# Optimization experiments

Hardware: AMD Instinct MI355X
Metric: run time of the kernel (lower is better)

## Reference

```python
import jax, jax.numpy as jnp
import numpy as np

B, C, H, W = 4, 256, 128, 128
D = 256            # attention hidden_dim (== C, so no output_proj)
HID = 1024         # mlp hidden = int(C * 4.0)
EPS = 1e-5


def setup_inputs() -> dict:
    key = jax.random.key(0)
    ks = jax.random.split(key, 16)
    s = 0.02
    return {
        "x": jax.random.normal(ks[0], (B, C, H, W), jnp.float32),
        "wq": jax.random.normal(ks[1], (C, D), jnp.float32) * s,
        "bq": jnp.zeros((D,), jnp.float32),
        "wk": jax.random.normal(ks[2], (C, D), jnp.float32) * s,
        "bk": jnp.zeros((D,), jnp.float32),
        "wv": jax.random.normal(ks[3], (C, D), jnp.float32) * s,
        "bv": jnp.zeros((D,), jnp.float32),
        "ln1_g": jnp.ones((C,), jnp.float32),
        "ln1_b": jnp.zeros((C,), jnp.float32),
        "ln2_g": jnp.ones((C,), jnp.float32),
        "ln2_b": jnp.zeros((C,), jnp.float32),
        "fc1_w": jax.random.normal(ks[4], (C, HID), jnp.float32) * s,
        "fc1_b": jnp.zeros((HID,), jnp.float32),
        "fc2_w": jax.random.normal(ks[5], (HID, C), jnp.float32) * s,
        "fc2_b": jnp.zeros((C,), jnp.float32),
    }


def _layernorm(x, g, b):
    m = jnp.mean(x, axis=-1, keepdims=True)
    v = jnp.mean(jnp.square(x - m), axis=-1, keepdims=True)
    return (x - m) * jax.lax.rsqrt(v + EPS) * g + b


def _neighborhoods(t):
    # t: [B,H,W,D] -> [B,H,W,9,D] 3x3 neighborhoods, zero-padded at borders
    tp = jnp.pad(t, ((0, 0), (1, 1), (1, 1), (0, 0)))
    h, w = t.shape[1], t.shape[2]
    return jnp.stack(
        [tp[:, dy:dy + h, dx:dx + w, :] for dy in range(3) for dx in range(3)],
        axis=3,
    )


def _valid_mask(h, w):
    # [H,W,9] bool: which of the 9 neighbors are inside the grid
    ys = jnp.arange(h)[:, None] * jnp.ones((1, w), jnp.int32)
    xs = jnp.arange(w)[None, :] * jnp.ones((h, 1), jnp.int32)
    top, bot = ys > 0, ys < h - 1
    lef, rig = xs > 0, xs < w - 1
    ones = jnp.ones((h, w), bool)
    return jnp.stack(
        [top & lef, top, top & rig, lef, ones, rig, bot & lef, bot, bot & rig],
        axis=-1,
    )


def reference(x, wq, bq, wk, bk, wv, bv, ln1_g, ln1_b, ln2_g, ln2_b,
              fc1_w, fc1_b, fc2_w, fc2_b):
    b_, c_, h_, w_ = x.shape
    xc = jnp.transpose(x, (0, 2, 3, 1))                    # [B,H,W,C]
    n1 = _layernorm(xc, ln1_g, ln1_b)
    q = n1 @ wq + bq                                       # [B,H,W,D]
    k = n1 @ wk + bk
    v = n1 @ wv + bv
    kn = _neighborhoods(k)                                  # [B,H,W,9,D]
    vn = _neighborhoods(v)
    scores = jnp.einsum('bhwd,bhwnd->bhwn', q, kn) / jnp.sqrt(jnp.float32(q.shape[-1]))
    mask = _valid_mask(h_, w_)                               # [H,W,9]
    scores = jnp.where(mask, scores, jnp.float32(-1e9))
    weights = jax.nn.softmax(scores, axis=-1)
    attn = jnp.einsum('bhwn,bhwnd->bhwd', weights, vn)       # [B,H,W,D]
    x1 = xc + attn                                           # residual 1
    n2 = _layernorm(x1, ln2_g, ln2_b)
    mlp = jax.nn.gelu(n2 @ fc1_w + fc1_b, approximate=False) @ fc2_w + fc2_b
    out = x1 + mlp
    return jnp.transpose(out, (0, 3, 1, 2))                  # [B,C,H,W]
```

## Files before the change

### kernel.cpp

```cpp
#include <hip/hip_runtime.h>
#include <hip/hip_bf16.h>
#include <math.h>

#define NPIX  65536
#define CCH   256
#define HWSZ  16384
#define WIDTH 128
#define HID   1024

typedef unsigned short u16;
typedef __bf16 bf16x8 __attribute__((ext_vector_type(8)));
typedef float  floatx4 __attribute__((ext_vector_type(4)));

__device__ __forceinline__ float bf2f(u16 u) {
  union { unsigned int i; float f; } c; c.i = ((unsigned int)u) << 16; return c.f;
}
__device__ __forceinline__ float bflo(unsigned int u) {
  union { unsigned int i; float f; } c; c.i = u << 16; return c.f;
}
__device__ __forceinline__ float bfhi(unsigned int u) {
  union { unsigned int i; float f; } c; c.i = u & 0xffff0000u; return c.f;
}
__device__ __forceinline__ u16 f2bf(float f) {
  union { float f; unsigned int i; } c; c.f = f;
  unsigned int x = c.i;
  x += 0x7fffu + ((x >> 16) & 1u);
  return (u16)(x >> 16);
}
__device__ __forceinline__ unsigned int packbf(float lo, float hi) {
  return ((unsigned int)f2bf(hi) << 16) | (unsigned int)f2bf(lo);
}
__device__ __forceinline__ float fast_rcp(float x) {
  float r; asm("v_rcp_f32 %0, %1" : "=v"(r) : "v"(x)); return r;
}
__device__ __forceinline__ float fast_exp2(float x) {
  float r; asm("v_exp_f32 %0, %1" : "=v"(r) : "v"(x)); return r;
}
__device__ __forceinline__ float gelu_fast(float x) {
  const float u = x * x;
  const float s = x * fmaf(0.1029432f, u, 2.3022082f);
  const float e = fast_exp2(-s);
  return x * fast_rcp(1.0f + e);
}

__device__ __forceinline__ void async16(const void* g, void* l) {
  __builtin_amdgcn_global_load_lds(
      (const __attribute__((address_space(1))) void*)g,
      (__attribute__((address_space(3))) void*)l, 16, 0, 0);
}

__global__ __launch_bounds__(256) void wfrag_kernel(
    const float* __restrict__ src, u16* __restrict__ dst, int N, int K) {
  const int tid = threadIdx.x;
  const int u = blockIdx.x * 4 + (tid >> 6);
  const int lane = tid & 63, quad = lane >> 4, l16 = lane & 15;
  const int K32 = K >> 5;
  const int g = u / K32, kb = u - g * K32;
  const int n = g * 16 + l16;
  const int k0 = kb * 32 + quad * 8;
  u16 tmp[8];
#pragma unroll
  for (int e = 0; e < 8; e++) tmp[e] = f2bf(src[(size_t)(k0 + e) * N + n]);
  *(bf16x8*)(dst + ((size_t)u * 64 + lane) * 8) = *(bf16x8*)tmp;
}

__global__ __launch_bounds__(256) void concat_bias_kernel(
    const float* __restrict__ bq, const float* __restrict__ bk,
    const float* __restrict__ bv, float* __restrict__ dst) {
  const int i = blockIdx.x * 256 + threadIdx.x;
  if (i < 256) dst[i] = bq[i];
  else if (i < 512) dst[i] = bk[i - 256];
  else if (i < 768) dst[i] = bv[i - 512];
}

__global__ __launch_bounds__(256) void ln1_kernel(
    const float* __restrict__ x, const float* __restrict__ g,
    const float* __restrict__ bb, u16* __restrict__ n1) {
  __shared__ float sx[32][257];
  __shared__ float sred[16][32];
  __shared__ float sm[32], sr[32];
  const int tx = threadIdx.x;
  const int p0 = blockIdx.x * 32;
  {
    const int pix = tx & 31, cpart = tx >> 5;
    const int p = p0 + pix;
    const int b = p >> 14, hw = p & (HWSZ - 1);
    const float* xb = x + ((size_t)b * CCH) * HWSZ + hw;
    float s = 0.f, s2 = 0.f;
#pragma unroll 4
    for (int i = 0; i < 32; i++) {
      const int c = cpart * 32 + i;
      const float v = xb[(size_t)c * HWSZ];
      sx[pix][c] = v;
      s += v; s2 += v * v;
    }
    sred[cpart][pix] = s; sred[8 + cpart][pix] = s2;
  }
  __syncthreads();
  if (tx < 32) {
    float s = 0.f, s2 = 0.f;
#pragma unroll
    for (int j = 0; j < 8; j++) { s += sred[j][tx]; s2 += sred[8 + j][tx]; }
    const float m = s * (1.0f / 256.0f);
    const float var = s2 * (1.0f / 256.0f) - m * m;
    sm[tx] = m; sr[tx] = rsqrtf(var + 1e-5f);
  }
  __syncthreads();
  const float gc = g[tx], bc = bb[tx];
#pragma unroll 4
  for (int i = 0; i < 32; i++) {
    const float v = (sx[i][tx] - sm[i]) * sr[i] * gc + bc;
    n1[(size_t)(p0 + i) * CCH + tx] = f2bf(v);
  }
}

__global__ __launch_bounds__(256) void res_ln2_kernel(
    const float* __restrict__ x, const u16* __restrict__ attn,
    const float* __restrict__ g, const float* __restrict__ bb,
    float* __restrict__ x1, u16* __restrict__ n2) {
  __shared__ float sx[32][257];
  __shared__ float sred[16][32];
  __shared__ float sm[32], sr[32];
  const int tx = threadIdx.x;
  const int p0 = blockIdx.x * 32;
  {
    const int pix = tx & 31, cpart = tx >> 5;
    const int p = p0 + pix;
    const int b = p >> 14, hw = p & (HWSZ - 1);
    const float* xb = x + ((size_t)b * CCH) * HWSZ + hw;
#pragma unroll 4
    for (int i = 0; i < 32; i++) {
      const int c = cpart * 32 + i;
      sx[pix][c] = xb[(size_t)c * HWSZ];
    }
  }
  __syncthreads();
#pragma unroll 4
  for (int i = 0; i < 32; i++) {
    const float v = sx[i][tx] + bf2f(attn[(size_t)(p0 + i) * CCH + tx]);
    sx[i][tx] = v;
    x1[(size_t)(p0 + i) * CCH + tx] = v;
  }
  __syncthreads();
  {
    const int pix = tx & 31, cpart = tx >> 5;
    float s = 0.f, s2 = 0.f;
#pragma unroll 4
    for (int i = 0; i < 32; i++) {
      const float v = sx[pix][cpart * 32 + i];
      s += v; s2 += v * v;
    }
    sred[cpart][pix] = s; sred[8 + cpart][pix] = s2;
  }
  __syncthreads();
  if (tx < 32) {
    float s = 0.f, s2 = 0.f;
#pragma unroll
    for (int j = 0; j < 8; j++) { s += sred[j][tx]; s2 += sred[8 + j][tx]; }
    const float m = s * (1.0f / 256.0f);
    const float var = s2 * (1.0f / 256.0f) - m * m;
    sm[tx] = m; sr[tx] = rsqrtf(var + 1e-5f);
  }
  __syncthreads();
  const float gc = g[tx], bc = bb[tx];
#pragma unroll 4
  for (int i = 0; i < 32; i++) {
    const float v = (sx[i][tx] - sm[i]) * sr[i] * gc + bc;
    n2[(size_t)(p0 + i) * CCH + tx] = f2bf(v);
  }
}

__global__ __launch_bounds__(256) void attn_kernel(
    const u16* __restrict__ qkv, u16* __restrict__ attn) {
  const int tid = threadIdx.x;
  const int wave = tid >> 6, lane = tid & 63;
  const int p = blockIdx.x * 4 + wave;
  const int hw = p & (HWSZ - 1);
  const int hh = hw >> 7, ww = hw & (WIDTH - 1);
  const u16* rowp = qkv + (size_t)p * 768 + lane * 4;
  const uint2 qr = *(const uint2*)rowp;
  const float qf0 = bflo(qr.x), qf1 = bfhi(qr.x);
  const float qf2 = bflo(qr.y), qf3 = bfhi(qr.y);
  float sc[9];
#pragma unroll
  for (int n = 0; n < 9; n++) {
    const int dy = n / 3 - 1, dx = n % 3 - 1;
    const int y = hh + dy, x2 = ww + dx;
    float s = -1e30f;
    if (y >= 0 && y < 128 && x2 >= 0 && x2 < 128) {
      const uint2 kr = *(const uint2*)(rowp + 256 + (dy * WIDTH + dx) * 768);
      float d = qf0 * bflo(kr.x) + qf1 * bfhi(kr.x)
              + qf2 * bflo(kr.y) + qf3 * bfhi(kr.y);
#pragma unroll
      for (int o = 32; o >= 1; o >>= 1) d += __shfl_xor(d, o, 64);
      s = d * 0.0625f;
    }
    sc[n] = s;
  }
  float mx = sc[0];
#pragma unroll
  for (int n = 1; n < 9; n++) mx = fmaxf(mx, sc[n]);
  float wgt[9], wsum = 0.f;
#pragma unroll
  for (int n = 0; n < 9; n++) { wgt[n] = __expf(sc[n] - mx); wsum += wgt[n]; }
  const float inv = 1.0f / wsum;
  float a0 = 0.f, a1 = 0.f, a2 = 0.f, a3 = 0.f;
#pragma unroll
  for (int n = 0; n < 9; n++) {
    const int dy = n / 3 - 1, dx = n % 3 - 1;
    const int y = hh + dy, x2 = ww + dx;
    if (y >= 0 && y < 128 && x2 >= 0 && x2 < 128) {
      const uint2 vr = *(const uint2*)(rowp + 512 + (dy * WIDTH + dx) * 768);
      const float wn = wgt[n] * inv;
      a0 += wn * bflo(vr.x); a1 += wn * bfhi(vr.x);
      a2 += wn * bflo(vr.y); a3 += wn * bfhi(vr.y);
    }
  }
  uint2 o;
  o.x = ((unsigned int)f2bf(a1) << 16) | (unsigned int)f2bf(a0);
  o.y = ((unsigned int)f2bf(a3) << 16) | (unsigned int)f2bf(a2);
  *(uint2*)(attn + (size_t)p * CCH + lane * 4) = o;
}

template <int NCH, int NST, int EPI>
__global__ __launch_bounds__(256, 3) void gemm_blds(
    const u16* __restrict__ A, const u16* __restrict__ wf,
    const float* __restrict__ bias, u16* __restrict__ outb) {
  __shared__ u16 sB[2][16384];
  const int tid  = threadIdx.x;
  const int wave = tid >> 6, lane = tid & 63;
  const int quad = lane >> 4, l16 = lane & 15;
  const int m0 = blockIdx.x * 128 + wave * 32;

  const u16* aRow = A + (size_t)(m0 + l16) * CCH + quad * 8;
  bf16x8 afr[2][8];
#pragma unroll
  for (int mi = 0; mi < 2; mi++)
#pragma unroll
    for (int ks = 0; ks < 8; ks++)
      afr[mi][ks] = *(const bf16x8*)(aRow + (size_t)mi * 16 * CCH + ks * 32);

  u16* rowPtr0 = outb + (size_t)(m0 + l16) * NST;
  u16* rowPtr1 = rowPtr0 + (size_t)16 * NST;

  auto stage = [&](int ch, int buf) {
    const u16* g = wf + (size_t)ch * 16384;
#pragma unroll
    for (int i = 0; i < 8; i++)
      async16(g + i * 2048 + tid * 8, &sB[buf][i * 2048 + tid * 8]);
  };

  stage(0, 0);
#pragma unroll 1
  for (int ch = 0; ch < NCH; ++ch) {
    __syncthreads();
    if (ch + 1 < NCH) stage(ch + 1, (ch + 1) & 1);
    const u16* sb = sB[ch & 1];
    floatx4 acc[2][4];
#pragma unroll
    for (int mi = 0; mi < 2; mi++)
#pragma unroll
      for (int gi = 0; gi < 4; gi++) acc[mi][gi] = (floatx4){0.f, 0.f, 0.f, 0.f};
#pragma unroll
    for (int ks = 0; ks < 8; ks++) {
      bf16x8 bfr[4];
#pragma unroll
      for (int gi = 0; gi < 4; gi++)
        bfr[gi] = *(const bf16x8*)&sb[(gi * 8 + ks) * 512 + lane * 8];
#pragma unroll
      for (int mi = 0; mi < 2; mi++)
#pragma unroll
        for (int gi = 0; gi < 4; gi++)
          acc[mi][gi] = __builtin_amdgcn_mfma_f32_16x16x32_bf16(
              bfr[gi], afr[mi][ks], acc[mi][gi], 0, 0, 0);
    }
#pragma unroll
    for (int gi = 0; gi < 4; gi++) {
      const int colb = ch * 64 + gi * 16 + quad * 4;
      const floatx4 bs4 = *(const floatx4*)&bias[colb];
#pragma unroll
      for (int mi = 0; mi < 2; mi++) {
        float v[4];
#pragma unroll
        for (int r = 0; r < 4; r++) {
          float val = acc[mi][gi][r] + bs4[r];
          if constexpr (EPI == 1) val = gelu_fast(val);
          v[r] = val;
        }
        uint2 w;
        w.x = packbf(v[0], v[1]);
        w.y = packbf(v[2], v[3]);
        *(uint2*)((mi == 0 ? rowPtr0 : rowPtr1) + colb) = w;
      }
    }
  }
}

__global__ __launch_bounds__(256, 2) void fc2_kernel(
    const u16* __restrict__ h, const u16* __restrict__ f2F,
    const float* __restrict__ bias, const float* __restrict__ x1,
    float* __restrict__ out) {
  __shared__ u16 sA[4][4096];
  __shared__ u16 sB[4][4096];
  const int tid  = threadIdx.x;
  const int wave = tid >> 6, lane = tid & 63;
  const int quad = lane >> 4, l16 = lane & 15;
  const int bx = blockIdx.x;
  const int mblk = (bx >> 1) * 128;
  const int nb = bx & 1;
  const int wgi = (wave >> 1) * 4;
  const int mloc = (wave & 1) * 64;

  auto stageA = [&](int kc, int buf) {
#pragma unroll
    for (int i = 0; i < 2; i++) {
      const int s = i * 256 + tid;
      async16(h + (size_t)(mblk + (s >> 2)) * HID + kc * 32 + (s & 3) * 8,
              &sA[buf][s * 8]);
    }
  };
  auto stageB = [&](int kc, int buf) {
#pragma unroll
    for (int i = 0; i < 2; i++) {
      const int s = i * 256 + tid;
      async16(f2F + (((size_t)(nb * 8 + (s >> 6)) * 32 + kc) << 9) + (s & 63) * 8,
              &sB[buf][s * 8]);
    }
  };

  floatx4 acc[4][4];
#pragma unroll
  for (int mi = 0; mi < 4; mi++)
#pragma unroll
    for (int gi = 0; gi < 4; gi++) acc[mi][gi] = (floatx4){0.f, 0.f, 0.f, 0.f};

  stageA(0, 0); stageB(0, 0);
  stageA(1, 1); stageB(1, 1);
#pragma unroll 1
  for (int kc = 0; kc < 32; ++kc) {
    if (kc < 31) asm volatile("s_waitcnt vmcnt(4)" ::: "memory");
    else         asm volatile("s_waitcnt vmcnt(0)" ::: "memory");
    __builtin_amdgcn_s_barrier();
    __builtin_amdgcn_sched_barrier(0);
    if (kc + 2 < 32) { stageA(kc + 2, (kc + 2) & 3); stageB(kc + 2, (kc + 2) & 3); }
    const u16* sa = sA[kc & 3];
    const u16* sb = sB[kc & 3];
    bf16x8 bfr[4], afr[4];
#pragma unroll
    for (int gi = 0; gi < 4; gi++)
      bfr[gi] = *(const bf16x8*)&sb[(wgi + gi) * 512 + lane * 8];
#pragma unroll
    for (int mi = 0; mi < 4; mi++)
      afr[mi] = *(const bf16x8*)&sa[(mloc + mi * 16 + l16) * 32 + quad * 8];
#pragma unroll
    for (int mi = 0; mi < 4; mi++)
#pragma unroll
      for (int gi = 0; gi < 4; gi++)
        acc[mi][gi] = __builtin_amdgcn_mfma_f32_16x16x32_bf16(
            afr[mi], bfr[gi], acc[mi][gi], 0, 0, 0);
  }

  const int m0 = mblk + mloc;
#pragma unroll
  for (int mi = 0; mi < 4; mi++)
#pragma unroll
    for (int gi = 0; gi < 4; gi++) {
      const int col = nb * 128 + (wgi + gi) * 16 + l16;
      const float bs = bias[col];
      const int row0 = m0 + mi * 16 + quad * 4;
      floatx4 vv;
#pragma unroll
      for (int r = 0; r < 4; r++)
        vv[r] = acc[mi][gi][r] + bs + x1[(size_t)(row0 + r) * CCH + col];
      *(floatx4*)&out[((size_t)((row0 >> 14) * CCH + col)) * HWSZ + (row0 & (HWSZ - 1))] = vv;
    }
}

extern "C" void kernel_launch(void* const* d_in, const int* in_sizes, int n_in,
                              void* d_out, int out_size, void* d_ws, size_t ws_size,
                              hipStream_t stream) {
  const float* x    = (const float*)d_in[0];
  const float* wq   = (const float*)d_in[1];
  const float* bq   = (const float*)d_in[2];
  const float* wk   = (const float*)d_in[3];
  const float* bk   = (const float*)d_in[4];
  const float* wv   = (const float*)d_in[5];
  const float* bv   = (const float*)d_in[6];
  const float* ln1g = (const float*)d_in[7];
  const float* ln1b = (const float*)d_in[8];
  const float* ln2g = (const float*)d_in[9];
  const float* ln2b = (const float*)d_in[10];
  const float* fc1w = (const float*)d_in[11];
  const float* fc1b = (const float*)d_in[12];
  const float* fc2w = (const float*)d_in[13];
  const float* fc2b = (const float*)d_in[14];
  float* out = (float*)d_out;

  char* ws = (char*)d_ws;
  const size_t MB = (size_t)1 << 20;
  float* x1   = (float*)(ws);
  u16* qkv    = (u16*)(ws + 64 * MB);
  u16* hbuf   = (u16*)(ws + 64 * MB);
  u16* n1     = (u16*)(ws + 160 * MB);
  u16* attnb  = n1;
  u16* n2     = (u16*)(ws + 192 * MB);
  u16* wqkvF  = (u16*)(ws + 224 * MB);
  u16* f1F    = wqkvF + 768 * 256;
  u16* f2F    = f1F + 1024 * 256;
  float* bqkv = (float*)(f2F + 256 * 1024);

  dim3 blk(256);
  wfrag_kernel<<<dim3(32),  blk, 0, stream>>>(wq,   wqkvF,          256, 256);
  wfrag_kernel<<<dim3(32),  blk, 0, stream>>>(wk,   wqkvF + 65536,  256, 256);
  wfrag_kernel<<<dim3(32),  blk, 0, stream>>>(wv,   wqkvF + 131072, 256, 256);
  wfrag_kernel<<<dim3(128), blk, 0, stream>>>(fc1w, f1F, 1024, 256);
  wfrag_kernel<<<dim3(128), blk, 0, stream>>>(fc2w, f2F, 256, 1024);
  concat_bias_kernel<<<dim3(3), blk, 0, stream>>>(bq, bk, bv, bqkv);

  ln1_kernel<<<NPIX / 32, blk, 0, stream>>>(x, ln1g, ln1b, n1);

  gemm_blds<12, 768, 0><<<dim3(NPIX / 128), blk, 0, stream>>>(n1, wqkvF, bqkv, qkv);

  attn_kernel<<<NPIX / 4, blk, 0, stream>>>(qkv, attnb);

  res_ln2_kernel<<<NPIX / 32, blk, 0, stream>>>(x, attnb, ln2g, ln2b, x1, n2);

  gemm_blds<16, 1024, 1><<<dim3(NPIX / 128), blk, 0, stream>>>(n2, f1F, fc1b, hbuf);

  fc2_kernel<<<dim3((NPIX / 128) * 2), blk, 0, stream>>>(hbuf, f2F, fc2b, x1, out);
}
```

Baseline: 460.0 us.

## Fuse fc1+GELU+fc2 into one MLP kernel keeping hidden activations on-chip

Replaces the separate fc1 GEMM (writing a bf16 hidden buffer to global memory) and fc2 GEMM with a single kernel. Each wave computes a 16-row slab of GELU(fc1) for 64 hidden columns per chunk, passes it through a small LDS scratch, and accumulates fc2 directly in registers, with fc2 weights read straight from global memory. This removes the round trip of the large hidden activation. It costs more registers, lower M-tile reuse of the weights (64 rows per block), and uncached global weight loads in the inner loop. It also changes the QKV GEMM's barrier to a partial vmcnt wait and hoists its bias load ahead of the next stage's prefetch.

```diff
diff --git a/kernel.cpp b/kernel.cpp
--- a/kernel.cpp
+++ b/kernel.cpp
@@ -253,8 +253,16 @@
   stage(0, 0);
 #pragma unroll 1
   for (int ch = 0; ch < NCH; ++ch) {
-    __syncthreads();
+    if (ch == 0) asm volatile("s_waitcnt vmcnt(0)" ::: "memory");
+    else         asm volatile("s_waitcnt vmcnt(8)" ::: "memory");
+    __builtin_amdgcn_s_barrier();
+    __builtin_amdgcn_sched_barrier(0);
+    floatx4 bs4pre[4];
+#pragma unroll
+    for (int gi = 0; gi < 4; gi++)
+      bs4pre[gi] = *(const floatx4*)&bias[ch * 64 + gi * 16 + quad * 4];
     if (ch + 1 < NCH) stage(ch + 1, (ch + 1) & 1);
+    __builtin_amdgcn_sched_barrier(0);
     const u16* sb = sB[ch & 1];
     floatx4 acc[2][4];
 #pragma unroll
@@ -277,7 +285,7 @@
 #pragma unroll
     for (int gi = 0; gi < 4; gi++) {
       const int colb = ch * 64 + gi * 16 + quad * 4;
-      const floatx4 bs4 = *(const floatx4*)&bias[colb];
+      const floatx4 bs4 = bs4pre[gi];
 #pragma unroll
       for (int mi = 0; mi < 2; mi++) {
         float v[4];
@@ -296,84 +304,102 @@
   }
 }
 
-__global__ __launch_bounds__(256, 2) void fc2_kernel(
-    const u16* __restrict__ h, const u16* __restrict__ f2F,
-    const float* __restrict__ bias, const float* __restrict__ x1,
+__global__ __launch_bounds__(256, 2) void mlp_kernel(
+    const u16* __restrict__ n2, const u16* __restrict__ f1F,
+    const u16* __restrict__ f2F, const float* __restrict__ b1,
+    const float* __restrict__ b2, const float* __restrict__ x1,
     float* __restrict__ out) {
-  __shared__ u16 sA[4][4096];
-  __shared__ u16 sB[4][4096];
+  __shared__ u16 sW[2][16384];
+  __shared__ __align__(16) u16 hx[4][16][72];
   const int tid  = threadIdx.x;
   const int wave = tid >> 6, lane = tid & 63;
   const int quad = lane >> 4, l16 = lane & 15;
-  const int bx = blockIdx.x;
-  const int mblk = (bx >> 1) * 128;
-  const int nb = bx & 1;
-  const int wgi = (wave >> 1) * 4;
-  const int mloc = (wave & 1) * 64;
-
-  auto stageA = [&](int kc, int buf) {
-#pragma unroll
-    for (int i = 0; i < 2; i++) {
-      const int s = i * 256 + tid;
-      async16(h + (size_t)(mblk + (s >> 2)) * HID + kc * 32 + (s & 3) * 8,
-              &sA[buf][s * 8]);
-    }
+  const int m0w = blockIdx.x * 64 + wave * 16;
+
+  const u16* aRow = n2 + (size_t)(m0w + l16) * CCH + quad * 8;
+  bf16x8 afr[8];
+#pragma unroll
+  for (int ks = 0; ks < 8; ks++)
+    afr[ks] = *(const bf16x8*)(aRow + ks * 32);
+
+  auto stageW1 = [&](int hc, int buf) {
+    const u16* g = f1F + (size_t)hc * 16384;
+#pragma unroll
+    for (int i = 0; i < 8; i++)
+      async16(g + i * 2048 + tid * 8, &sW[buf][i * 2048 + tid * 8]);
   };
-  auto stageB = [&](int kc, int buf) {
-#pragma unroll
-    for (int i = 0; i < 2; i++) {
-      const int s = i * 256 + tid;
-      async16(f2F + (((size_t)(nb * 8 + (s >> 6)) * 32 + kc) << 9) + (s & 63) * 8,
-              &sB[buf][s * 8]);
-    }
-  };
-
-  floatx4 acc[4][4];
-#pragma unroll
-  for (int mi = 0; mi < 4; mi++)
-#pragma unroll
-    for (int gi = 0; gi < 4; gi++) acc[mi][gi] = (floatx4){0.f, 0.f, 0.f, 0.f};
-
-  stageA(0, 0); stageB(0, 0);
-  stageA(1, 1); stageB(1, 1);
+
+  const u16* w2Base = f2F + lane * 8;
+
+  floatx4 acc2[16];
+#pragma unroll
+  for (int gi2 = 0; gi2 < 16; gi2++) acc2[gi2] = (floatx4){0.f, 0.f, 0.f, 0.f};
+
+  stageW1(0, 0);
 #pragma unroll 1
-  for (int kc = 0; kc < 32; ++kc) {
-    if (kc < 31) asm volatile("s_waitcnt vmcnt(4)" ::: "memory");
-    else         asm volatile("s_waitcnt vmcnt(0)" ::: "memory");
-    __builtin_amdgcn_s_barrier();
-    __builtin_amdgcn_sched_barrier(0);
-    if (kc + 2 < 32) { stageA(kc + 2, (kc + 2) & 3); stageB(kc + 2, (kc + 2) & 3); }
-    const u16* sa = sA[kc & 3];
-    const u16* sb = sB[kc & 3];
-    bf16x8 bfr[4], afr[4];
+  for (int hc = 0; hc < 16; ++hc) {
+    __syncthreads();
+    bf16x8 w2a[16];
+#pragma unroll
+    for (int gi2 = 0; gi2 < 16; gi2++)
+      w2a[gi2] = *(const bf16x8*)(w2Base + (((size_t)gi2 * 32 + hc * 2) << 9));
+    if (hc + 1 < 16) stageW1(hc + 1, (hc + 1) & 1);
+    floatx4 bs1[4];
 #pragma unroll
     for (int gi = 0; gi < 4; gi++)
-      bfr[gi] = *(const bf16x8*)&sb[(wgi + gi) * 512 + lane * 8];
-#pragma unroll
-    for (int mi = 0; mi < 4; mi++)
-      afr[mi] = *(const bf16x8*)&sa[(mloc + mi * 16 + l16) * 32 + quad * 8];
-#pragma unroll
-    for (int mi = 0; mi < 4; mi++)
+      bs1[gi] = *(const floatx4*)&b1[hc * 64 + gi * 16 + quad * 4];
+    const u16* sb = sW[hc & 1];
+    floatx4 acc1[4];
+#pragma unroll
+    for (int gi = 0; gi < 4; gi++) acc1[gi] = (floatx4){0.f, 0.f, 0.f, 0.f};
+#pragma unroll
+    for (int ks = 0; ks < 8; ks++) {
+      bf16x8 bfr[4];
 #pragma unroll
       for (int gi = 0; gi < 4; gi++)
-        acc[mi][gi] = __builtin_amdgcn_mfma_f32_16x16x32_bf16(
-            afr[mi], bfr[gi], acc[mi][gi], 0, 0, 0);
-  }
-
-  const int m0 = mblk + mloc;
-#pragma unroll
-  for (int mi = 0; mi < 4; mi++)
+        bfr[gi] = *(const bf16x8*)&sb[(gi * 8 + ks) * 512 + lane * 8];
+#pragma unroll
+      for (int gi = 0; gi < 4; gi++)
+        acc1[gi] = __builtin_amdgcn_mfma_f32_16x16x32_bf16(
+            bfr[gi], afr[ks], acc1[gi], 0, 0, 0);
+    }
 #pragma unroll
     for (int gi = 0; gi < 4; gi++) {
-      const int col = nb * 128 + (wgi + gi) * 16 + l16;
-      const float bs = bias[col];
-      const int row0 = m0 + mi * 16 + quad * 4;
-      floatx4 vv;
-#pragma unroll
-      for (int r = 0; r < 4; r++)
-        vv[r] = acc[mi][gi][r] + bs + x1[(size_t)(row0 + r) * CCH + col];
-      *(floatx4*)&out[((size_t)((row0 >> 14) * CCH + col)) * HWSZ + (row0 & (HWSZ - 1))] = vv;
-    }
+      float v[4];
+#pragma unroll
+      for (int r = 0; r < 4; r++) v[r] = gelu_fast(acc1[gi][r] + bs1[gi][r]);
+      uint2 w;
+      w.x = packbf(v[0], v[1]);
+      w.y = packbf(v[2], v[3]);
+      *(uint2*)&hx[wave][l16][gi * 16 + quad * 4] = w;
+    }
+    bf16x8 hfrag[2];
+#pragma unroll
+    for (int ks2 = 0; ks2 < 2; ks2++)
+      hfrag[ks2] = *(const bf16x8*)&hx[wave][l16][ks2 * 32 + quad * 8];
+#pragma unroll
+    for (int gi2 = 0; gi2 < 16; gi2++)
+      acc2[gi2] = __builtin_amdgcn_mfma_f32_16x16x32_bf16(
+          hfrag[0], w2a[gi2], acc2[gi2], 0, 0, 0);
+#pragma unroll
+    for (int gi2 = 0; gi2 < 16; gi2++) {
+      const bf16x8 w2b = *(const bf16x8*)(w2Base + (((size_t)gi2 * 32 + hc * 2 + 1) << 9));
+      acc2[gi2] = __builtin_amdgcn_mfma_f32_16x16x32_bf16(
+          hfrag[1], w2b, acc2[gi2], 0, 0, 0);
+    }
+  }
+
+#pragma unroll
+  for (int gi2 = 0; gi2 < 16; gi2++) {
+    const int col = gi2 * 16 + l16;
+    const float bs = b2[col];
+    const int row0 = m0w + quad * 4;
+    floatx4 vv;
+#pragma unroll
+    for (int r = 0; r < 4; r++)
+      vv[r] = acc2[gi2][r] + bs + x1[(size_t)(row0 + r) * CCH + col];
+    *(floatx4*)&out[((size_t)((row0 >> 14) * CCH + col)) * HWSZ + (row0 & (HWSZ - 1))] = vv;
+  }
 }
 
 extern "C" void kernel_launch(void* const* d_in, const int* in_sizes, int n_in,
@@ -400,7 +426,6 @@
   const size_t MB = (size_t)1 << 20;
   float* x1   = (float*)(ws);
   u16* qkv    = (u16*)(ws + 64 * MB);
-  u16* hbuf   = (u16*)(ws + 64 * MB);
   u16* n1     = (u16*)(ws + 160 * MB);
   u16* attnb  = n1;
   u16* n2     = (u16*)(ws + 192 * MB);
@@ -425,7 +450,5 @@
 
   res_ln2_kernel<<<NPIX / 32, blk, 0, stream>>>(x, attnb, ln2g, ln2b, x1, n2);
 
-  gemm_blds<16, 1024, 1><<<dim3(NPIX / 128), blk, 0, stream>>>(n2, f1F, fc1b, hbuf);
-
-  fc2_kernel<<<dim3((NPIX / 128) * 2), blk, 0, stream>>>(hbuf, f2F, fc2b, x1, out);
-}
+  mlp_kernel<<<dim3(NPIX / 64), blk, 0, stream>>>(n2, f1F, f2F, fc1b, fc2b, x1, out);
+}
```

New measurement: 498.0 us. 8.3% more time.
